# Kernel optimization log

Measured on AMD Instinct MI355X. Metric: run time of the kernel, lower is better.

## Reference

```python
import jax, jax.numpy as jnp
import numpy as np

N_NODES = 100000
N_EDGES = 2000000
IN_C = 30
OUT_C = 10
HID = 4 * OUT_C      # 40
D1 = 2 * OUT_C       # 20
D2 = OUT_C           # 10
N_CLASSES = 3
K_SAMPLE = 8


def setup_inputs() -> dict:
    key = jax.random.key(0)
    ks = jax.random.split(key, 24)
    inp = {
        'x': jax.random.normal(ks[0], (N_NODES, IN_C), dtype=jnp.float32),
        'edge_index': jax.random.randint(ks[1], (2, N_EDGES), 0, N_NODES, dtype=jnp.int64),
        'edge_attr': jax.random.uniform(ks[2], (N_EDGES,), dtype=jnp.float32),
        'label': 1,
        # gcn1
        'W1': jax.random.normal(ks[3], (IN_C, HID), dtype=jnp.float32) * (1.0 / np.sqrt(IN_C)),
        'b1': jnp.zeros((HID,), jnp.float32),
        'ln1_w': jnp.ones((HID,), jnp.float32),
        'ln1_b': jnp.zeros((HID,), jnp.float32),
        # gcn2
        'W2': jax.random.normal(ks[4], (HID, HID), dtype=jnp.float32) * (1.0 / np.sqrt(HID)),
        'b2': jnp.zeros((HID,), jnp.float32),
        'ln2_w': jnp.ones((HID,), jnp.float32),
        'ln2_b': jnp.zeros((HID,), jnp.float32),
        # fnn
        'Wf': jax.random.normal(ks[5], (HID, D1), dtype=jnp.float32) * (1.0 / np.sqrt(HID)),
        'bf': jnp.zeros((D1,), jnp.float32),
        # attention (tanh / sigmoid branches + concat)
        'Wt': jax.random.normal(ks[6], (D1, D2), dtype=jnp.float32) * (1.0 / np.sqrt(D1)),
        'bt': jnp.zeros((D2,), jnp.float32),
        'Ws': jax.random.normal(ks[7], (D1, D2), dtype=jnp.float32) * (1.0 / np.sqrt(D1)),
        'bs': jnp.zeros((D2,), jnp.float32),
        'Wc': jax.random.normal(ks[8], (D2, 1), dtype=jnp.float32) * (1.0 / np.sqrt(D2)),
        'bc': jnp.zeros((1,), jnp.float32),
        # bag classifier
        'Wcls': jax.random.normal(ks[9], (D1, N_CLASSES), dtype=jnp.float32) * (1.0 / np.sqrt(D1)),
        'bcls': jnp.zeros((N_CLASSES,), jnp.float32),
        # per-class cell-scale classifiers, stacked [n_classes, D1, 2]
        'Wcell': jax.random.normal(ks[10], (N_CLASSES, D1, 2), dtype=jnp.float32) * (1.0 / np.sqrt(D1)),
        'bcell': jnp.zeros((N_CLASSES, 2), jnp.float32),
    }
    return inp


def _layernorm(x, w, b, eps=1e-5):
    m = jnp.mean(x, axis=-1, keepdims=True)
    v = jnp.var(x, axis=-1, keepdims=True)
    return (x - m) * jax.lax.rsqrt(v + eps) * w + b


def _gcn(x, W, b, src, dst, ew, n):
    # PyG GCNConv: add self-loops (weight 1), symmetric norm, aggregate at dst
    h = x @ W                                              # [N, F]
    deg = jax.ops.segment_sum(ew, dst, num_segments=n) + 1.0
    dinv = jnp.where(deg > 0, jax.lax.rsqrt(deg), 0.0)     # [N]
    norm = dinv[src] * ew * dinv[dst]                      # [E]
    agg = jax.ops.segment_sum(h[src] * norm[:, None], dst, num_segments=n)
    agg = agg + h * (dinv * dinv)[:, None]                 # self-loop term
    return agg + b


def _forward(x, edge_attr, W1, b1, ln1_w, ln1_b, W2, b2, ln2_w, ln2_b,
             Wf, bf, Wt, bt, Ws, bs, Wc, bc, Wcls, bcls, Wcell, bcell,
             edge_index, label):
    src, dst = edge_index[0], edge_index[1]
    n = x.shape[0]
    x1 = jax.nn.selu(_layernorm(_gcn(x, W1, b1, src, dst, edge_attr, n), ln1_w, ln1_b))
    x2 = jax.nn.selu(_layernorm(_gcn(x1, W2, b2, src, dst, edge_attr, n), ln2_w, ln2_b))
    x3 = jax.nn.selu(x2 @ Wf + bf)                         # [N, D1] == x_out
    # gated tanh*sigmoid attention
    gate = jnp.tanh(x3 @ Wt + bt) * jax.nn.sigmoid(x3 @ Ws + bs)
    A = (gate @ Wc + bc).T                                 # [1, N]
    A = jax.nn.softmax(A, axis=1)
    # cell-scale eval for the true class (one-hot label selects exactly one)
    a_row = A[-1]                                          # [N]
    _, idx_p = jax.lax.top_k(a_row, K_SAMPLE)
    _, idx_n = jax.lax.top_k(-a_row, K_SAMPLE)
    all_cells = jnp.concatenate([x3[idx_p], x3[idx_n]], axis=0)   # [2K, D1]
    logits_c = all_cells @ Wcell[label] + bcell[label]            # [2K, 2]
    targets = jnp.concatenate([jnp.ones((K_SAMPLE,), jnp.int32),
                               jnp.zeros((K_SAMPLE,), jnp.int32)])
    # SmoothTop1SVM (tau=1, alpha=1): mean( logsumexp(s + Delta) - s_y )
    delta = 1.0 - jax.nn.one_hot(targets, 2, dtype=logits_c.dtype)
    s_y = jnp.take_along_axis(logits_c, targets[:, None], axis=1)[:, 0]
    cell_loss = jnp.mean(jax.nn.logsumexp(logits_c + delta, axis=1) - s_y)
    # bag-level prediction
    x_pooled = A @ x3                                      # [1, D1]
    logits = x_pooled @ Wcls + bcls                        # [1, n_classes]
    Y_prob = jax.nn.softmax(logits, axis=1)
    Y_hat = jnp.argmax(logits, axis=1)[:, None]
    return logits, Y_prob, Y_hat, A, x3, cell_loss


def reference(x, edge_index, edge_attr, label, W1, b1, ln1_w, ln1_b, W2, b2,
              ln2_w, ln2_b, Wf, bf, Wt, bt, Ws, bs, Wc, bc, Wcls, bcls,
              Wcell, bcell):
    return _forward(x, edge_attr, W1, b1, ln1_w, ln1_b, W2, b2, ln2_w, ln2_b,
                    Wf, bf, Wt, bt, Ws, bs, Wc, bc, Wcls, bcls, Wcell, bcell,
                    edge_index, label)
```

## Files before the change

kernel.cpp:

```cpp
#include <hip/hip_runtime.h>
#include <hip/hip_bf16.h>
#include <math.h>

typedef __hip_bfloat16 bf16;

__device__ __forceinline__ float tof(bf16 v){ return __bfloat162float(v); }
__device__ __forceinline__ bf16  tob(float v){ return __float2bfloat16(v); }

__device__ __forceinline__ float sane(float v){
  return (v == v && v > -1e30f && v < 1e30f) ? v : 0.f;
}
__device__ __forceinline__ float ldf(const void* p, size_t i, bool f32){
  float v = f32 ? ((const float*)p)[i] : tof(((const bf16*)p)[i]);
  return sane(v);
}
__device__ __forceinline__ void stf(void* p, size_t i, float v, bool f32){
  if (f32) ((float*)p)[i] = v; else ((bf16*)p)[i] = tob(v);
}
__device__ __forceinline__ bool is_f32(const unsigned* __restrict__ dt){
  return dt[0] == 0x3F800000u;
}
__device__ __forceinline__ int clampi(int v, int hi){
  return ((unsigned)v < (unsigned)hi) ? v : 0;
}
__device__ __forceinline__ float selu_f(float x){
  const float sc = 1.0507009873554805f, al = 1.6732632423543772f;
  return x > 0.f ? sc * x : sc * al * (expf(x) - 1.0f);
}
__device__ __forceinline__ void unpack8(uint4 u, float* f){
  f[0]=__uint_as_float(u.x<<16); f[1]=__uint_as_float(u.x&0xFFFF0000u);
  f[2]=__uint_as_float(u.y<<16); f[3]=__uint_as_float(u.y&0xFFFF0000u);
  f[4]=__uint_as_float(u.z<<16); f[5]=__uint_as_float(u.z&0xFFFF0000u);
  f[6]=__uint_as_float(u.w<<16); f[7]=__uint_as_float(u.w&0xFFFF0000u);
}
__device__ __forceinline__ void unpack4(uint2 u, float* f){
  f[0]=__uint_as_float(u.x<<16); f[1]=__uint_as_float(u.x&0xFFFF0000u);
  f[2]=__uint_as_float(u.y<<16); f[3]=__uint_as_float(u.y&0xFFFF0000u);
}
__device__ __forceinline__ unsigned pack2(float a, float b){
  unsigned short ua, ub;
  bf16 ta = tob(a), tb = tob(b);
  __builtin_memcpy(&ua, &ta, 2);
  __builtin_memcpy(&ub, &tb, 2);
  return (unsigned)ua | ((unsigned)ub << 16);
}

__global__ void k_zero(float* __restrict__ p, int n){
  int i = blockIdx.x * blockDim.x + threadIdx.x;
  int stride = gridDim.x * blockDim.x;
  for (; i < n; i += stride) p[i] = 0.f;
}

__device__ __forceinline__ bool idx_is64(const int* __restrict__ raw){
  return ((raw[1] | raw[3] | raw[5] | raw[7] | raw[9] | raw[11]) == 0);
}
__device__ __forceinline__ void edge_at(const int* __restrict__ raw, int E, int e,
                                        bool w64, int N, int& s, int& d){
  int sv, dv;
  if (w64){ sv = raw[2 * e]; dv = raw[2 * (E + e)]; }
  else    { sv = raw[e];     dv = raw[E + e]; }
  s = clampi(sv, N); d = clampi(dv, N);
}

__global__ void k_cnt_rank(const int* __restrict__ raw, int* __restrict__ cnt,
                           int* __restrict__ rank, int E, int N){
  int e = blockIdx.x * blockDim.x + threadIdx.x;
  if (e >= E) return;
  bool w64 = idx_is64(raw);
  int s, d; edge_at(raw, E, e, w64, N, s, d);
  rank[e] = atomicAdd(&cnt[d], 1);
}

__global__ void k_scan_block(const int* __restrict__ cnt, int* __restrict__ bsum, int N){
  __shared__ int s[256];
  int base = blockIdx.x * 1024;
  int acc = 0;
  for (int k = threadIdx.x; k < 1024; k += 256){
    int i = base + k;
    acc += (i < N) ? cnt[i] : 0;
  }
  s[threadIdx.x] = acc; __syncthreads();
  for (int w = 128; w > 0; w >>= 1){
    if (threadIdx.x < w) s[threadIdx.x] += s[threadIdx.x + w];
    __syncthreads();
  }
  if (threadIdx.x == 0) bsum[blockIdx.x] = s[0];
}

__global__ void k_scan_partials(int* __restrict__ bsum, int B, int* __restrict__ rowpN, int E){
  __shared__ int s[256];
  int run = 0;
  for (int t0 = 0; t0 < B; t0 += 256){
    int i = t0 + threadIdx.x;
    int v = (i < B) ? bsum[i] : 0;
    s[threadIdx.x] = v;
    __syncthreads();
    for (int o = 1; o < 256; o <<= 1){
      int add = (threadIdx.x >= o) ? s[threadIdx.x - o] : 0;
      __syncthreads();
      s[threadIdx.x] += add;
      __syncthreads();
    }
    int incl = s[threadIdx.x];
    int total = s[255];
    __syncthreads();
    if (i < B) bsum[i] = run + incl - v;
    run += total;
    __syncthreads();
  }
  if (threadIdx.x == 0) rowpN[0] = E;
}

__global__ void k_scan_final(const int* __restrict__ cnt, const int* __restrict__ bsum,
                             int* __restrict__ rowp, int N){
  __shared__ int s[256];
  int t = threadIdx.x;
  int base = bsum[blockIdx.x];
  int i0 = blockIdx.x * 1024 + t * 4;
  int v0=0,v1=0,v2=0,v3=0;
  if (i0+0 < N) v0 = cnt[i0+0];
  if (i0+1 < N) v1 = cnt[i0+1];
  if (i0+2 < N) v2 = cnt[i0+2];
  if (i0+3 < N) v3 = cnt[i0+3];
  int sum = v0+v1+v2+v3;
  s[t] = sum; __syncthreads();
  for (int o = 1; o < 256; o <<= 1){
    int add = (t >= o) ? s[t - o] : 0;
    __syncthreads();
    s[t] += add;
    __syncthreads();
  }
  int off = base + s[t] - sum;
  if (i0+0 < N){ rowp[i0+0]=off; off+=v0; }
  if (i0+1 < N){ rowp[i0+1]=off; off+=v1; }
  if (i0+2 < N){ rowp[i0+2]=off; off+=v2; }
  if (i0+3 < N){ rowp[i0+3]=off; off+=v3; }
}

__global__ void k_place(const int* __restrict__ raw, const void* __restrict__ ea,
                        const unsigned* __restrict__ dt, const int* __restrict__ rank,
                        const int* __restrict__ rowp, int2* __restrict__ ep, int E, int N){
  int e = blockIdx.x * blockDim.x + threadIdx.x;
  if (e >= E) return;
  bool f32 = is_f32(dt);
  bool w64 = idx_is64(raw);
  int s, d; edge_at(raw, E, e, w64, N, s, d);
  float w = ldf(ea, e, f32);
  int pos = rowp[d] + rank[e];
  if ((unsigned)pos < (unsigned)E)
    ep[pos] = make_int2(s, __float_as_int(w));
}

__global__ void k_dinv_csr(const int* __restrict__ rowp, const int2* __restrict__ ep,
                           float* __restrict__ dinv, int N, int E){
  int n = blockIdx.x * blockDim.x + threadIdx.x;
  if (n >= N) return;
  int beg = rowp[n], end = rowp[n + 1];
  if (beg < 0) beg = 0;
  if (end > E) end = E;
  float s = 0.f;
  for (int j = beg; j < end; j++) s += sane(__int_as_float(ep[j].y));
  float dv = s + 1.0f;
  dinv[n] = (dv > 0.f) ? rsqrtf(dv) : 0.f;
}

__global__ void k_mm1(const void* __restrict__ X, const void* __restrict__ W,
                      const unsigned* __restrict__ dt,
                      bf16* __restrict__ H, int N, int Nx){
  bool f32 = is_f32(dt);
  __shared__ float w[30 * 40];
  __shared__ float xs[256 * 30];
  for (int i = threadIdx.x; i < 30 * 40; i += 256) w[i] = ldf(W, i, f32);
  int base = blockIdx.x * 256;
  int rows = Nx - base; if (rows > 256) rows = 256; if (rows < 0) rows = 0;
  int nelem = rows * 30;
  size_t gbase = (size_t)base * 30;
  for (int i = threadIdx.x; i < nelem; i += 256) xs[i] = ldf(X, gbase + i, f32);
  __syncthreads();
  int n = base + threadIdx.x;
  if (n >= N) return;
  float acc[40];
  #pragma unroll
  for (int j = 0; j < 40; j++) acc[j] = 0.f;
  if (threadIdx.x < rows){
    const float* xr = &xs[threadIdx.x * 30];
    for (int i = 0; i < 30; i++){
      float xi = xr[i];
      #pragma unroll
      for (int j = 0; j < 40; j++) acc[j] += xi * w[i * 40 + j];
    }
  } else {
    for (int i = 0; i < 30; i++){
      float xi = ldf(X, i, f32);
      #pragma unroll
      for (int j = 0; j < 40; j++) acc[j] += xi * w[i * 40 + j];
    }
  }
  uint4 ob[5];
  unsigned* ou = (unsigned*)ob;
  #pragma unroll
  for (int q = 0; q < 20; q++) ou[q] = pack2(acc[2*q], acc[2*q+1]);
  uint4* op = (uint4*)(H + (size_t)n * 40);
  #pragma unroll
  for (int q = 0; q < 5; q++) op[q] = ob[q];
}

__global__ void k_mm2(const bf16* __restrict__ X, const void* __restrict__ W,
                      const unsigned* __restrict__ dt,
                      bf16* __restrict__ H, int N){
  bool f32 = is_f32(dt);
  __shared__ float w[40 * 40];
  for (int i = threadIdx.x; i < 40 * 40; i += 256) w[i] = ldf(W, i, f32);
  __syncthreads();
  int n = blockIdx.x * blockDim.x + threadIdx.x;
  if (n >= N) return;
  float acc[40];
  #pragma unroll
  for (int j = 0; j < 40; j++) acc[j] = 0.f;
  const uint4* xp = (const uint4*)(X + (size_t)n * 40);
  #pragma unroll
  for (int q = 0; q < 5; q++){
    uint4 u = xp[q];
    float f[8]; unpack8(u, f);
    #pragma unroll
    for (int k = 0; k < 8; k++){
      float xi = f[k];
      int i = q * 8 + k;
      #pragma unroll
      for (int j = 0; j < 40; j++) acc[j] += xi * w[i * 40 + j];
    }
  }
  uint4 ob[5];
  unsigned* ou = (unsigned*)ob;
  #pragma unroll
  for (int q = 0; q < 20; q++) ou[q] = pack2(acc[2*q], acc[2*q+1]);
  uint4* op = (uint4*)(H + (size_t)n * 40);
  #pragma unroll
  for (int q = 0; q < 5; q++) op[q] = ob[q];
}

__global__ void k_gather(const int* __restrict__ rowp, const int2* __restrict__ ep,
                         const bf16* __restrict__ h, const float* __restrict__ dinv,
                         const void* __restrict__ b, const void* __restrict__ lw,
                         const void* __restrict__ lb, const unsigned* __restrict__ dt,
                         bf16* __restrict__ xout, int N, int E){
  int n = blockIdx.x * blockDim.x + threadIdx.x;
  if (n >= N) return;
  bool f32 = is_f32(dt);
  float dn = dinv[n];
  float acc[40];
  #pragma unroll
  for (int f = 0; f < 40; f++) acc[f] = 0.f;
  int beg = rowp[n], end = rowp[n + 1];
  if (beg < 0) beg = 0;
  if (end > E) end = E;
  for (int j = beg; j < end; j++){
    int2 p = ep[j];
    int s = clampi(p.x, N);
    float w = dinv[s] * __int_as_float(p.y) * dn;
    const uint4* hp = (const uint4*)(h + (size_t)s * 40);
    #pragma unroll
    for (int q = 0; q < 5; q++){
      uint4 u = hp[q];
      float f[8]; unpack8(u, f);
      #pragma unroll
      for (int k = 0; k < 8; k++) acc[q * 8 + k] += f[k] * w;
    }
  }
  float di2 = dn * dn;
  const uint4* hp = (const uint4*)(h + (size_t)n * 40);
  float v[40]; float m = 0.f;
  #pragma unroll
  for (int q = 0; q < 5; q++){
    uint4 u = hp[q];
    float f[8]; unpack8(u, f);
    #pragma unroll
    for (int k = 0; k < 8; k++){
      int idx = q * 8 + k;
      v[idx] = sane(acc[idx]) + f[k] * di2 + ldf(b, idx, f32);
      m += v[idx];
    }
  }
  m *= (1.0f / 40.0f);
  float var = 0.f;
  #pragma unroll
  for (int f = 0; f < 40; f++){ float d = v[f] - m; var += d * d; }
  var *= (1.0f / 40.0f);
  float inv = rsqrtf(var + 1e-5f);
  float y[40];
  #pragma unroll
  for (int f = 0; f < 40; f++)
    y[f] = sane(selu_f((v[f] - m) * inv * ldf(lw, f, f32) + ldf(lb, f, f32)));
  uint4 ob[5];
  unsigned* ou = (unsigned*)ob;
  #pragma unroll
  for (int q = 0; q < 20; q++) ou[q] = pack2(y[2*q], y[2*q+1]);
  uint4* op = (uint4*)(xout + (size_t)n * 40);
  #pragma unroll
  for (int q = 0; q < 5; q++) op[q] = ob[q];
}

__global__ void k_head(const bf16* __restrict__ x2,
                       const void* __restrict__ Wf, const void* __restrict__ bfv,
                       const void* __restrict__ Wt, const void* __restrict__ bt,
                       const void* __restrict__ Ws, const void* __restrict__ bs,
                       const void* __restrict__ Wc, const void* __restrict__ bc,
                       const unsigned* __restrict__ dt,
                       bf16* __restrict__ x3ws, float* __restrict__ alog, int N){
  bool f32 = is_f32(dt);
  __shared__ float wf[800], bff[20], wt[200], btt[10], wss[200], bss[10], wc[10], bcc[1];
  for (int i = threadIdx.x; i < 800; i += blockDim.x) wf[i] = ldf(Wf, i, f32);
  for (int i = threadIdx.x; i < 200; i += blockDim.x){
    wt[i] = ldf(Wt, i, f32); wss[i] = ldf(Ws, i, f32);
  }
  if (threadIdx.x < 20) bff[threadIdx.x] = ldf(bfv, threadIdx.x, f32);
  if (threadIdx.x < 10){ btt[threadIdx.x] = ldf(bt, threadIdx.x, f32);
                         bss[threadIdx.x] = ldf(bs, threadIdx.x, f32);
                         wc[threadIdx.x]  = ldf(Wc, threadIdx.x, f32); }
  if (threadIdx.x == 0) bcc[0] = ldf(bc, 0, f32);
  __syncthreads();
  int n = blockIdx.x * blockDim.x + threadIdx.x;
  if (n >= N) return;
  float r[40];
  const uint4* xp = (const uint4*)(x2 + (size_t)n * 40);
  #pragma unroll
  for (int q = 0; q < 5; q++){
    uint4 u = xp[q];
    unpack8(u, &r[q * 8]);
  }
  float x3r[20];
  #pragma unroll
  for (int j = 0; j < 20; j++){
    float acc = bff[j];
    for (int i = 0; i < 40; i++) acc += r[i] * wf[i * 20 + j];
    x3r[j] = sane(selu_f(acc));
  }
  uint2 ob[5];
  unsigned* ou = (unsigned*)ob;
  #pragma unroll
  for (int q = 0; q < 10; q++) ou[q] = pack2(x3r[2*q], x3r[2*q+1]);
  uint2* op = (uint2*)(x3ws + (size_t)n * 20);
  #pragma unroll
  for (int q = 0; q < 5; q++) op[q] = ob[q];
  float a = bcc[0];
  #pragma unroll
  for (int j = 0; j < 10; j++){
    float zt = btt[j], zs = bss[j];
    for (int i = 0; i < 20; i++){ zt += x3r[i] * wt[i * 10 + j]; zs += x3r[i] * wss[i * 10 + j]; }
    float g = tanhf(zt) * (1.0f / (1.0f + expf(-zs)));
    a += g * wc[j];
  }
  alog[n] = sane(a);
}

__global__ void k_copy_x3(const bf16* __restrict__ x3ws, const unsigned* __restrict__ dt,
                          void* __restrict__ out, size_t off, int total){
  bool f32 = is_f32(dt);
  int i = blockIdx.x * blockDim.x + threadIdx.x;
  int stride = gridDim.x * blockDim.x;
  for (; i < total; i += stride) stf(out, off + i, tof(x3ws[i]), f32);
}

__global__ void k_msum(const float* __restrict__ a, float2* __restrict__ part, int n){
  __shared__ float sm[256], sl[256];
  int t = threadIdx.x;
  float m = -1e30f, l = 0.f;
  for (int i = blockIdx.x * blockDim.x + t; i < n; i += gridDim.x * blockDim.x){
    float v = sane(a[i]);
    if (v > m){ l = l * expf(m - v) + 1.f; m = v; }
    else        l += expf(v - m);
  }
  sm[t] = m; sl[t] = l; __syncthreads();
  for (int w = 128; w > 0; w >>= 1){
    if (t < w){
      float m2 = sm[t+w], l2 = sl[t+w];
      float mm = fmaxf(sm[t], m2);
      sl[t] = sl[t] * expf(sm[t] - mm) + l2 * expf(m2 - mm);
      sm[t] = mm;
    }
    __syncthreads();
  }
  if (t == 0) part[blockIdx.x] = make_float2(sm[0], sl[0]);
}

__global__ void k_msum_fin(const float2* __restrict__ part, float* __restrict__ scal,
                           float* __restrict__ pooled){
  __shared__ float sm[256], sl[256];
  int t = threadIdx.x;
  float2 p = part[t];
  sm[t] = p.x; sl[t] = p.y; __syncthreads();
  for (int w = 128; w > 0; w >>= 1){
    if (t < w){
      float m2 = sm[t+w], l2 = sl[t+w];
      float mm = fmaxf(sm[t], m2);
      sl[t] = sl[t] * expf(sm[t] - mm) + l2 * expf(m2 - mm);
      sm[t] = mm;
    }
    __syncthreads();
  }
  if (t == 0){ scal[0] = sm[0]; scal[1] = sl[0]; }
  if (t < 20) pooled[t] = 0.f;
}

__global__ void k_writeA(const float* __restrict__ alog, const bf16* __restrict__ x3ws,
                         const float* __restrict__ scal,
                         const unsigned* __restrict__ dt,
                         void* __restrict__ out, size_t a_off,
                         float* __restrict__ pooled, int N){
  bool f32 = is_f32(dt);
  float gmax = scal[0];
  float sum  = scal[1];
  float inv  = (sum > 0.f) ? 1.0f / sum : 0.f;
  float acc[20];
  #pragma unroll
  for (int j = 0; j < 20; j++) acc[j] = 0.f;
  for (int i = blockIdx.x * blockDim.x + threadIdx.x; i < N; i += gridDim.x * blockDim.x){
    float a = expf(sane(alog[i]) - gmax) * inv;
    stf(out, a_off + i, a, f32);
    const uint2* xr = (const uint2*)(x3ws + (size_t)i * 20);
    #pragma unroll
    for (int q = 0; q < 5; q++){
      float f[4]; unpack4(xr[q], f);
      #pragma unroll
      for (int k = 0; k < 4; k++) acc[q * 4 + k] += a * f[k];
    }
  }
  __shared__ float s[20];
  if (threadIdx.x < 20) s[threadIdx.x] = 0.f;
  __syncthreads();
  #pragma unroll
  for (int j = 0; j < 20; j++) atomicAdd(&s[j], acc[j]);
  __syncthreads();
  if (threadIdx.x < 20) atomicAdd(&pooled[threadIdx.x], s[threadIdx.x]);
}

__global__ void k_topk1(const float* __restrict__ a, int N,
                        float* __restrict__ cvp, int* __restrict__ cip,
                        float* __restrict__ cvn, int* __restrict__ cin){
  const int T = 256, K = 8;
  __shared__ float sv[T * K];
  __shared__ int   si[T * K];
  __shared__ float rv[T];
  __shared__ int   ri[T];
  __shared__ int   rs[T];
  int t = threadIdx.x;
  float tv[K]; int ti[K]; float bv[K]; int bi[K];
  #pragma unroll
  for (int k = 0; k < K; k++){ tv[k] = -1e38f; ti[k] = 0x7ffffff;
                               bv[k] =  1e38f; bi[k] = 0x7ffffff; }
  for (int i = blockIdx.x * T + t; i < N; i += gridDim.x * T){
    float v = sane(a[i]);
    if (v > tv[K-1]){
      int p = K - 1;
      while (p > 0 && v > tv[p-1]){ tv[p] = tv[p-1]; ti[p] = ti[p-1]; p--; }
      tv[p] = v; ti[p] = i;
    }
    if (v < bv[K-1]){
      int p = K - 1;
      while (p > 0 && v < bv[p-1]){ bv[p] = bv[p-1]; bi[p] = bi[p-1]; p--; }
      bv[p] = v; bi[p] = i;
    }
  }
  for (int k = 0; k < K; k++){ sv[t*K+k] = tv[k]; si[t*K+k] = ti[k]; }
  __syncthreads();
  for (int round = 0; round < K; round++){
    float bvv = -1e38f; int bii = 0x7ffffff; int bslot = 0;
    for (int k = 0; k < K; k++){
      float v = sv[t*K+k]; int ii = si[t*K+k];
      if (v > bvv || (v == bvv && ii < bii)){ bvv = v; bii = ii; bslot = t*K+k; }
    }
    rv[t] = bvv; ri[t] = bii; rs[t] = bslot;
    __syncthreads();
    for (int w = T/2; w > 0; w >>= 1){
      if (t < w){
        float v2 = rv[t+w]; int i2 = ri[t+w];
        if (v2 > rv[t] || (v2 == rv[t] && i2 < ri[t])){ rv[t]=v2; ri[t]=i2; rs[t]=rs[t+w]; }
      }
      __syncthreads();
    }
    if (t == 0){ cvp[blockIdx.x*K + round] = rv[0]; cip[blockIdx.x*K + round] = ri[0];
                 sv[rs[0]] = -1e38f; }
    __syncthreads();
  }
  for (int k = 0; k < K; k++){ sv[t*K+k] = bv[k]; si[t*K+k] = bi[k]; }
  __syncthreads();
  for (int round = 0; round < K; round++){
    float bvv = 1e38f; int bii = 0x7ffffff; int bslot = 0;
    for (int k = 0; k < K; k++){
      float v = sv[t*K+k]; int ii = si[t*K+k];
      if (v < bvv || (v == bvv && ii < bii)){ bvv = v; bii = ii; bslot = t*K+k; }
    }
    rv[t] = bvv; ri[t] = bii; rs[t] = bslot;
    __syncthreads();
    for (int w = T/2; w > 0; w >>= 1){
      if (t < w){
        float v2 = rv[t+w]; int i2 = ri[t+w];
        if (v2 < rv[t] || (v2 == rv[t] && i2 < ri[t])){ rv[t]=v2; ri[t]=i2; rs[t]=rs[t+w]; }
      }
      __syncthreads();
    }
    if (t == 0){ cvn[blockIdx.x*K + round] = rv[0]; cin[blockIdx.x*K + round] = ri[0];
                 sv[rs[0]] = 1e38f; }
    __syncthreads();
  }
}

__global__ void k_topk2(const float* __restrict__ cvp, const int* __restrict__ cip,
                        const float* __restrict__ cvn, const int* __restrict__ cin,
                        int* __restrict__ idxp, int* __restrict__ idxn, int M){
  const int T = 256, CAP = 1024, PER = CAP / T;
  __shared__ float sv[CAP];
  __shared__ int   si[CAP];
  __shared__ float rv[T];
  __shared__ int   ri[T];
  __shared__ int   rs[T];
  int t = threadIdx.x;
  for (int i = t; i < CAP; i += T){
    sv[i] = (i < M) ? cvp[i] : -1e38f;
    si[i] = (i < M) ? cip[i] : 0x7ffffff;
  }
  __syncthreads();
  for (int round = 0; round < 8; round++){
    float bvv = -1e38f; int bii = 0x7ffffff; int bslot = t * PER;
    for (int k = 0; k < PER; k++){
      float v = sv[t*PER+k]; int ii = si[t*PER+k];
      if (v > bvv || (v == bvv && ii < bii)){ bvv = v; bii = ii; bslot = t*PER+k; }
    }
    rv[t] = bvv; ri[t] = bii; rs[t] = bslot;
    __syncthreads();
    for (int w = T/2; w > 0; w >>= 1){
      if (t < w){
        float v2 = rv[t+w]; int i2 = ri[t+w];
        if (v2 > rv[t] || (v2 == rv[t] && i2 < ri[t])){ rv[t]=v2; ri[t]=i2; rs[t]=rs[t+w]; }
      }
      __syncthreads();
    }
    if (t == 0){ idxp[round] = ri[0]; sv[rs[0]] = -1e38f; }
    __syncthreads();
  }
  for (int i = t; i < CAP; i += T){
    sv[i] = (i < M) ? cvn[i] : 1e38f;
    si[i] = (i < M) ? cin[i] : 0x7ffffff;
  }
  __syncthreads();
  for (int round = 0; round < 8; round++){
    float bvv = 1e38f; int bii = 0x7ffffff; int bslot = t * PER;
    for (int k = 0; k < PER; k++){
      float v = sv[t*PER+k]; int ii = si[t*PER+k];
      if (v < bvv || (v == bvv && ii < bii)){ bvv = v; bii = ii; bslot = t*PER+k; }
    }
    rv[t] = bvv; ri[t] = bii; rs[t] = bslot;
    __syncthreads();
    for (int w = T/2; w > 0; w >>= 1){
      if (t < w){
        float v2 = rv[t+w]; int i2 = ri[t+w];
        if (v2 < rv[t] || (v2 == rv[t] && i2 < ri[t])){ rv[t]=v2; ri[t]=i2; rs[t]=rs[t+w]; }
      }
      __syncthreads();
    }
    if (t == 0){ idxn[round] = ri[0]; sv[rs[0]] = 1e38f; }
    __syncthreads();
  }
}

__global__ void k_final(const float* __restrict__ pooled,
                        const void* __restrict__ Wcls, const void* __restrict__ bcls,
                        const void* __restrict__ Wcell, const void* __restrict__ bcell,
                        const int* __restrict__ label_p, const bf16* __restrict__ x3ws,
                        const int* __restrict__ idxp, const int* __restrict__ idxn,
                        const unsigned* __restrict__ dt,
                        void* __restrict__ out, int N){
  if (threadIdx.x != 0 || blockIdx.x != 0) return;
  bool f32 = is_f32(dt);
  float lg[3];
  for (int c = 0; c < 3; c++){
    float acc = ldf(bcls, c, f32);
    for (int j = 0; j < 20; j++) acc += sane(pooled[j]) * ldf(Wcls, j * 3 + c, f32);
    lg[c] = sane(acc);
  }
  float m = fmaxf(lg[0], fmaxf(lg[1], lg[2]));
  float e0 = expf(lg[0]-m), e1 = expf(lg[1]-m), e2 = expf(lg[2]-m);
  float es = e0 + e1 + e2;
  int yhat = 0;
  if (lg[1] > lg[yhat]) yhat = 1;
  if (lg[2] > lg[yhat]) yhat = 2;
  stf(out, 0, lg[0], f32); stf(out, 1, lg[1], f32); stf(out, 2, lg[2], f32);
  stf(out, 3, e0/es, f32); stf(out, 4, e1/es, f32); stf(out, 5, e2/es, f32);
  stf(out, 6, (float)yhat, f32);
  int lw0 = label_p[0];
  int label;
  if ((unsigned)lw0 < 3u) label = lw0;
  else if (lw0 == 0x3F800000 || lw0 == 0x3F803F80) label = 1;
  else if (lw0 == 0x40000000 || lw0 == 0x40004000) label = 2;
  else label = 0;
  float w0[20], w1[20];
  for (int j = 0; j < 20; j++){
    w0[j] = ldf(Wcell, (size_t)label * 40 + j*2 + 0, f32);
    w1[j] = ldf(Wcell, (size_t)label * 40 + j*2 + 1, f32);
  }
  float b0 = ldf(bcell, (size_t)label * 2 + 0, f32);
  float b1 = ldf(bcell, (size_t)label * 2 + 1, f32);
  float loss = 0.f;
  for (int i = 0; i < 16; i++){
    int node = clampi((i < 8) ? idxp[i] : idxn[i-8], N);
    const bf16* xr = x3ws + (size_t)node * 20;
    float l0 = b0, l1 = b1;
    for (int j = 0; j < 20; j++){ float xv = tof(xr[j]); l0 += xv * w0[j]; l1 += xv * w1[j]; }
    int tgt = (i < 8) ? 1 : 0;
    float a0 = l0 + ((tgt == 0) ? 0.f : 1.f);
    float a1 = l1 + ((tgt == 1) ? 0.f : 1.f);
    float mm = fmaxf(a0, a1);
    float lse = mm + logf(expf(a0-mm) + expf(a1-mm));
    float sy = tgt ? l1 : l0;
    loss += lse - sy;
  }
  stf(out, (size_t)7 + N + (size_t)20 * N, sane(loss * (1.0f / 16.0f)), f32);
}

extern "C" void kernel_launch(void* const* d_in, const int* in_sizes, int n_in,
                              void* d_out, int out_size, void* d_ws, size_t ws_size,
                              hipStream_t stream) {
  const int N = (out_size - 8) / 21;
  if (N <= 0) return;
  const int Nx = (in_sizes[0] / 30 < N) ? (in_sizes[0] / 30) : N;
  int E = in_sizes[1] / 2;
  if (in_sizes[2] < E) E = in_sizes[2];
  if (E < 6) return;

  const void* x    = d_in[0];
  const int*  eraw = (const int*)d_in[1];
  const void* ea   = d_in[2];
  const int*  lbl  = (const int*)d_in[3];
  const void* W1   = d_in[4];
  const void* b1   = d_in[5];
  const unsigned* dt = (const unsigned*)d_in[6];
  const void* ln1w = d_in[6];
  const void* ln1b = d_in[7];
  const void* W2   = d_in[8];
  const void* b2   = d_in[9];
  const void* ln2w = d_in[10];
  const void* ln2b = d_in[11];
  const void* Wf   = d_in[12];
  const void* bfv  = d_in[13];
  const void* Wt   = d_in[14];
  const void* bt   = d_in[15];
  const void* Ws   = d_in[16];
  const void* bs   = d_in[17];
  const void* Wc   = d_in[18];
  const void* bc   = d_in[19];
  const void* Wcls = d_in[20];
  const void* bcls = d_in[21];
  const void* Wcell= d_in[22];
  const void* bcell= d_in[23];

  auto align16 = [](size_t v){ return (v + 15) & ~(size_t)15; };
  size_t hA_bytes = (size_t)N * 40 * 2;
  size_t rank_bytes = (size_t)E * 4;
  size_t regA = hA_bytes > rank_bytes ? hA_bytes : rank_bytes;
  size_t off = 0;
  char* ws = (char*)d_ws;
  bf16* hA    = (bf16*)(ws + off);
  int*  rank  = (int*)(ws + off);  off = align16(off + regA);
  bf16* xB    = (bf16*)(ws + off); off = align16(off + (size_t)N * 40 * 2);
  int2* epack = (int2*)(ws + off); off = align16(off + (size_t)E * 8);
  int*  rowp  = (int*)(ws + off);  off = align16(off + (size_t)(N + 1) * 4);
  int*  cnt   = (int*)(ws + off);  off = align16(off + (size_t)N * 4);
  int*  bsum  = (int*)(ws + off);  off = align16(off + 4096 * 4);
  float* dinv = (float*)(ws + off); off = align16(off + (size_t)N * 4);
  float* alog = (float*)(ws + off); off = align16(off + (size_t)N * 4);
  float2* part2 = (float2*)(ws + off); off = align16(off + 256 * 8);
  float* scal = (float*)(ws + off); off = align16(off + 2 * 4);
  float* pooled = (float*)(ws + off); off = align16(off + 20 * 4);
  int*   idxp = (int*)(ws + off); off = align16(off + 8 * 4);
  int*   idxn = (int*)(ws + off); off = align16(off + 8 * 4);
  float* cvp  = (float*)(ws + off); off = align16(off + 1024 * 4);
  int*   cip  = (int*)(ws + off);   off = align16(off + 1024 * 4);
  float* cvn  = (float*)(ws + off); off = align16(off + 1024 * 4);
  int*   cin  = (int*)(ws + off);   off = align16(off + 1024 * 4);
  if (off > ws_size) return;
  bf16* x3ws = hA;

  const int TB = 256;
  const int gN = (N + TB - 1) / TB;
  const int gE = (E + TB - 1) / TB;
  const int SB = (N + 1023) / 1024;
  const int TP = 128;

  k_zero<<<gN, TB, 0, stream>>>((float*)cnt, N);
  k_cnt_rank<<<gE, TB, 0, stream>>>(eraw, cnt, rank, E, N);
  k_scan_block<<<SB, TB, 0, stream>>>(cnt, bsum, N);
  k_scan_partials<<<1, TB, 0, stream>>>(bsum, SB, rowp + N, E);
  k_scan_final<<<SB, TB, 0, stream>>>(cnt, bsum, rowp, N);
  k_place<<<gE, TB, 0, stream>>>(eraw, ea, dt, rank, rowp, epack, E, N);
  k_dinv_csr<<<gN, TB, 0, stream>>>(rowp, epack, dinv, N, E);

  k_mm1<<<gN, TB, 0, stream>>>(x, W1, dt, hA, N, Nx);
  k_gather<<<gN, TB, 0, stream>>>(rowp, epack, hA, dinv, b1, ln1w, ln1b, dt, xB, N, E);

  k_mm2<<<gN, TB, 0, stream>>>(xB, W2, dt, hA, N);
  k_gather<<<gN, TB, 0, stream>>>(rowp, epack, hA, dinv, b2, ln2w, ln2b, dt, xB, N, E);

  k_head<<<gN, TB, 0, stream>>>(xB, Wf, bfv, Wt, bt, Ws, bs, Wc, bc, dt,
                                x3ws, alog, N);
  k_copy_x3<<<2048, TB, 0, stream>>>(x3ws, dt, d_out, (size_t)7 + N, 20 * N);

  k_msum<<<256, TB, 0, stream>>>(alog, part2, N);
  k_msum_fin<<<1, TB, 0, stream>>>(part2, scal, pooled);
  k_writeA<<<256, TB, 0, stream>>>(alog, x3ws, scal, dt, d_out, (size_t)7, pooled, N);

  k_topk1<<<TP, TB, 0, stream>>>(alog, N, cvp, cip, cvn, cin);
  k_topk2<<<1, TB, 0, stream>>>(cvp, cip, cvn, cin, idxp, idxn, TP * 8);
  k_final<<<1, 64, 0, stream>>>(pooled, Wcls, bcls, Wcell, bcell, lbl,
                                x3ws, idxp, idxn, dt, d_out, N);
}
```

Baseline: 651.5 us.

## Gather GCN neighbors with one wavefront per node and pre-scaled edge weights

Rewrites the GCN aggregation kernel from one thread per node to one 64-lane wavefront per node, where lanes 0-39 each own one feature and LayerNorm statistics come from shuffle reductions. A new pass multiplies each CSR edge weight by dinv of its source once, so both gather launches skip that per-edge lookup. The aim is to spread high-degree rows across lanes, load bf16 feature rows coalesced instead of each thread walking its own neighbor list, and cut per-thread register pressure. In exchange 24 of 64 lanes sit idle, every lane redundantly loads the edge records, and an extra edge-sized kernel pass is added.

Result: slower. 681.2 us (+4.6%).

```diff
diff --git a/kernel.cpp b/kernel.cpp
--- a/kernel.cpp
+++ b/kernel.cpp
@@ -164,6 +164,16 @@
   dinv[n] = (dv > 0.f) ? rsqrtf(dv) : 0.f;
 }
 
+__global__ void k_premul(int2* __restrict__ ep, const float* __restrict__ dinv,
+                         int E, int N){
+  int i = blockIdx.x * blockDim.x + threadIdx.x;
+  if (i >= E) return;
+  int2 p = ep[i];
+  int s = clampi(p.x, N);
+  float w = dinv[s] * sane(__int_as_float(p.y));
+  ep[i] = make_int2(s, __float_as_int(w));
+}
+
 __global__ void k_mm1(const void* __restrict__ X, const void* __restrict__ W,
                       const unsigned* __restrict__ dt,
                       bf16* __restrict__ H, int N, int Nx){
@@ -244,60 +254,53 @@
                          const void* __restrict__ b, const void* __restrict__ lw,
                          const void* __restrict__ lb, const unsigned* __restrict__ dt,
                          bf16* __restrict__ xout, int N, int E){
-  int n = blockIdx.x * blockDim.x + threadIdx.x;
+  int n = (blockIdx.x * blockDim.x + threadIdx.x) >> 6;
+  int lane = threadIdx.x & 63;
   if (n >= N) return;
   bool f32 = is_f32(dt);
+  bool act = lane < 40;
   float dn = dinv[n];
-  float acc[40];
-  #pragma unroll
-  for (int f = 0; f < 40; f++) acc[f] = 0.f;
   int beg = rowp[n], end = rowp[n + 1];
   if (beg < 0) beg = 0;
   if (end > E) end = E;
-  for (int j = beg; j < end; j++){
+  float acc = 0.f;
+  int j = beg;
+  for (; j + 3 < end; j += 4){
+    int2 p0 = ep[j+0], p1 = ep[j+1], p2 = ep[j+2], p3 = ep[j+3];
+    int s0 = clampi(p0.x, N), s1 = clampi(p1.x, N);
+    int s2 = clampi(p2.x, N), s3 = clampi(p3.x, N);
+    float h0 = 0.f, h1 = 0.f, h2 = 0.f, h3 = 0.f;
+    if (act){
+      h0 = tof(h[(size_t)s0 * 40 + lane]);
+      h1 = tof(h[(size_t)s1 * 40 + lane]);
+      h2 = tof(h[(size_t)s2 * 40 + lane]);
+      h3 = tof(h[(size_t)s3 * 40 + lane]);
+    }
+    acc += h0 * __int_as_float(p0.y) + h1 * __int_as_float(p1.y)
+         + h2 * __int_as_float(p2.y) + h3 * __int_as_float(p3.y);
+  }
+  for (; j < end; j++){
     int2 p = ep[j];
     int s = clampi(p.x, N);
-    float w = dinv[s] * __int_as_float(p.y) * dn;
-    const uint4* hp = (const uint4*)(h + (size_t)s * 40);
-    #pragma unroll
-    for (int q = 0; q < 5; q++){
-      uint4 u = hp[q];
-      float f[8]; unpack8(u, f);
-      #pragma unroll
-      for (int k = 0; k < 8; k++) acc[q * 8 + k] += f[k] * w;
-    }
-  }
-  float di2 = dn * dn;
-  const uint4* hp = (const uint4*)(h + (size_t)n * 40);
-  float v[40]; float m = 0.f;
-  #pragma unroll
-  for (int q = 0; q < 5; q++){
-    uint4 u = hp[q];
-    float f[8]; unpack8(u, f);
-    #pragma unroll
-    for (int k = 0; k < 8; k++){
-      int idx = q * 8 + k;
-      v[idx] = sane(acc[idx]) + f[k] * di2 + ldf(b, idx, f32);
-      m += v[idx];
-    }
-  }
-  m *= (1.0f / 40.0f);
-  float var = 0.f;
-  #pragma unroll
-  for (int f = 0; f < 40; f++){ float d = v[f] - m; var += d * d; }
-  var *= (1.0f / 40.0f);
-  float inv = rsqrtf(var + 1e-5f);
-  float y[40];
-  #pragma unroll
-  for (int f = 0; f < 40; f++)
-    y[f] = sane(selu_f((v[f] - m) * inv * ldf(lw, f, f32) + ldf(lb, f, f32)));
-  uint4 ob[5];
-  unsigned* ou = (unsigned*)ob;
-  #pragma unroll
-  for (int q = 0; q < 20; q++) ou[q] = pack2(y[2*q], y[2*q+1]);
-  uint4* op = (uint4*)(xout + (size_t)n * 40);
-  #pragma unroll
-  for (int q = 0; q < 5; q++) op[q] = ob[q];
+    float hv = act ? tof(h[(size_t)s * 40 + lane]) : 0.f;
+    acc += hv * __int_as_float(p.y);
+  }
+  acc *= dn;
+  float hself = act ? tof(h[(size_t)n * 40 + lane]) : 0.f;
+  float v = act ? (sane(acc) + hself * dn * dn + ldf(b, lane, f32)) : 0.f;
+  float sum = v;
+  #pragma unroll
+  for (int o = 1; o < 64; o <<= 1) sum += __shfl_xor(sum, o);
+  float m = sum * (1.0f / 40.0f);
+  float d = act ? (v - m) : 0.f;
+  float sq = d * d;
+  #pragma unroll
+  for (int o = 1; o < 64; o <<= 1) sq += __shfl_xor(sq, o);
+  float inv = rsqrtf(sq * (1.0f / 40.0f) + 1e-5f);
+  if (act){
+    float y = sane(selu_f(d * inv * ldf(lw, lane, f32) + ldf(lb, lane, f32)));
+    xout[(size_t)n * 40 + lane] = tob(y);
+  }
 }
 
 __global__ void k_head(const bf16* __restrict__ x2,
@@ -683,6 +686,7 @@
   const int TB = 256;
   const int gN = (N + TB - 1) / TB;
   const int gE = (E + TB - 1) / TB;
+  const int gW = (N + 3) / 4;
   const int SB = (N + 1023) / 1024;
   const int TP = 128;
 
@@ -693,12 +697,13 @@
   k_scan_final<<<SB, TB, 0, stream>>>(cnt, bsum, rowp, N);
   k_place<<<gE, TB, 0, stream>>>(eraw, ea, dt, rank, rowp, epack, E, N);
   k_dinv_csr<<<gN, TB, 0, stream>>>(rowp, epack, dinv, N, E);
+  k_premul<<<gE, TB, 0, stream>>>(epack, dinv, E, N);
 
   k_mm1<<<gN, TB, 0, stream>>>(x, W1, dt, hA, N, Nx);
-  k_gather<<<gN, TB, 0, stream>>>(rowp, epack, hA, dinv, b1, ln1w, ln1b, dt, xB, N, E);
+  k_gather<<<gW, TB, 0, stream>>>(rowp, epack, hA, dinv, b1, ln1w, ln1b, dt, xB, N, E);
 
   k_mm2<<<gN, TB, 0, stream>>>(xB, W2, dt, hA, N);
-  k_gather<<<gN, TB, 0, stream>>>(rowp, epack, hA, dinv, b2, ln2w, ln2b, dt, xB, N, E);
+  k_gather<<<gW, TB, 0, stream>>>(rowp, epack, hA, dinv, b2, ln2w, ln2b, dt, xB, N, E);
 
   k_head<<<gN, TB, 0, stream>>>(xB, Wf, bfv, Wt, bt, Ws, bs, Wc, bc, dt,
                                 x3ws, alog, N);
```
